# Performance work log

Hardware: AMD Instinct MI355X
Metric: run time of the kernel (lower is better)

Reference implementation:

```python
import jax, jax.numpy as jnp
import numpy as np

B, E, LC, LE, D = 32, 8, 256, 512, 256   # batch, evi_num, claim_len, evidence_len, emb_dim
OUT, H = 128, 1                          # attention hidden dim, head_num
NEG = -1e18


def setup_inputs() -> dict:
    key = jax.random.key(0)
    ks = jax.random.split(key, 8)
    claim = jax.random.normal(ks[0], (B, E, LC, D), jnp.float32)
    evidence = jax.random.normal(ks[1], (B, E, LE, D), jnp.float32)
    claim_len_mask = jax.random.randint(ks[2], (B, E, 1, LC), 0, 2).astype(jnp.int32)
    evidence_len_mask = jax.random.randint(ks[3], (B, E, 1, LE), 0, 2).astype(jnp.int32)
    s2d = 1.0 / np.sqrt(2 * D)
    so = 1.0 / np.sqrt(OUT)
    W1 = jax.random.normal(ks[4], (2 * D, OUT), jnp.float32) * s2d  # torch W1.weight.T
    w2 = jax.random.normal(ks[5], (OUT, H), jnp.float32) * so
    W2 = jax.random.normal(ks[6], (2 * D, OUT), jnp.float32) * s2d
    w1 = jax.random.normal(ks[7], (OUT, H), jnp.float32) * so
    return {"claim": claim, "claim_len_mask": claim_len_mask,
            "evidence": evidence, "evidence_len_mask": evidence_len_mask,
            "W1": W1, "w2": w2, "W2": W2, "w1": w1}


def _pooled_attend(seq, seq_mask, pooled, W, w):
    # seq: (B,E,L,D), pooled: (B,E,1,D), W: (2D,OUT), w: (OUT,H)
    # cat([seq, pooled_expanded]) @ W  ==  seq @ W[:D] + pooled @ W[D:]  (broadcast)
    h = jnp.tanh(seq @ W[:D] + pooled @ W[D:])          # (B,E,L,OUT)
    att = h @ w                                          # (B,E,L,H)
    mask = jnp.swapaxes(seq_mask, -1, -2).astype(bool)   # (B,E,L,1), broadcast over H
    att = jnp.where(mask, att, NEG)
    scores = jax.nn.softmax(att, axis=-2)                # softmax over L
    out = jnp.einsum('belh,beld->behd', scores, seq)     # (B,E,H,D)
    return out.reshape(out.shape[0], out.shape[1], 1, -1)  # (B,E,1,H*D)


def reference(claim, claim_len_mask, evidence, evidence_len_mask, W1, w2, W2, w1):
    c_mean = jnp.mean(claim, axis=-2, keepdims=True)     # (B,E,1,D)
    e_hat = _pooled_attend(evidence, evidence_len_mask, c_mean, W1, w2)
    e_mean = jnp.mean(evidence, axis=-2, keepdims=True)  # (B,E,1,D)
    c_hat = _pooled_attend(claim, claim_len_mask, e_mean, W2, w1)
    return c_hat, e_hat
```

## Files before the change

kernel.cpp:

```cpp
#include <hip/hip_runtime.h>
#include <hip/hip_bf16.h>
#include <math.h>

#define BE   256
#define DIM  256
#define OUTD 128
#define LCL  256
#define LEV  512
#define NEGV -1e18f

typedef short  bf16x8  __attribute__((ext_vector_type(8)));
typedef float  floatx4 __attribute__((ext_vector_type(4)));

union BF1 { __hip_bfloat16 h; unsigned short u; };
union BF2 { __hip_bfloat162 h; unsigned int u; };

__device__ __forceinline__ float fast_tanh(float x) {
    float xc = fminf(fmaxf(x, -15.f), 15.f);
    float e = __expf(2.f * xc);
    return (e - 1.f) * __builtin_amdgcn_rcpf(e + 1.f);
}

__global__ __launch_bounds__(512) void k_meanbias(
    const float* __restrict__ claim, const float* __restrict__ evidence,
    const float* __restrict__ W1, const float* __restrict__ W2,
    float* __restrict__ bias_e, float* __restrict__ bias_c,
    unsigned short* __restrict__ WT1, unsigned short* __restrict__ WT2)
{
    const int bid = blockIdx.x;
    const int t = threadIdx.x;
    if (bid >= BE) {
        const int side = bid - BE;
        const float* W = side ? W2 : W1;
        unsigned short* WT = side ? WT2 : WT1;
        for (int i = t; i < OUTD * DIM; i += 512) {
            const int d = i & (DIM - 1);
            const int n = i >> 8;
            BF1 c; c.h = __float2bfloat16(W[(size_t)d * OUTD + n]);
            WT[n * DIM + d] = c.u;
        }
        return;
    }
    const int pair = bid;
    const int d4 = t & 63, rg = t >> 6;
    __shared__ float4 smc[8][64];
    __shared__ float4 sme[8][64];
    __shared__ float mc[DIM], me[DIM];
    __shared__ float sb[2][2][OUTD];

    const float4* c4 = (const float4*)(claim + (size_t)pair * LCL * DIM);
    const float4* e4 = (const float4*)(evidence + (size_t)pair * LEV * DIM);
    float4 ac = make_float4(0.f, 0.f, 0.f, 0.f);
    float4 ae = make_float4(0.f, 0.f, 0.f, 0.f);
#pragma unroll 4
    for (int r = rg; r < LCL; r += 8) {
        const float4 v = c4[r * 64 + d4];
        ac.x += v.x; ac.y += v.y; ac.z += v.z; ac.w += v.w;
    }
#pragma unroll 4
    for (int r = rg; r < LEV; r += 8) {
        const float4 v = e4[r * 64 + d4];
        ae.x += v.x; ae.y += v.y; ae.z += v.z; ae.w += v.w;
    }
    smc[rg][d4] = ac; sme[rg][d4] = ae;
    __syncthreads();
    if (t < 64) {
        float4 s = make_float4(0.f, 0.f, 0.f, 0.f);
#pragma unroll
        for (int j = 0; j < 8; ++j) {
            const float4 v = smc[j][t];
            s.x += v.x; s.y += v.y; s.z += v.z; s.w += v.w;
        }
        ((float4*)mc)[t] = make_float4(s.x * (1.f / LCL), s.y * (1.f / LCL),
                                       s.z * (1.f / LCL), s.w * (1.f / LCL));
    } else if (t < 128) {
        const int u = t - 64;
        float4 s = make_float4(0.f, 0.f, 0.f, 0.f);
#pragma unroll
        for (int j = 0; j < 8; ++j) {
            const float4 v = sme[j][u];
            s.x += v.x; s.y += v.y; s.z += v.z; s.w += v.w;
        }
        ((float4*)me)[u] = make_float4(s.x * (1.f / LEV), s.y * (1.f / LEV),
                                       s.z * (1.f / LEV), s.w * (1.f / LEV));
    }
    __syncthreads();
    const int side = t >> 8, o = t & 127, dh = (t >> 7) & 1;
    const float* W = side ? W2 : W1;
    const float* m = side ? me : mc;
    float s = 0.f;
#pragma unroll 8
    for (int i = 0; i < 128; ++i) {
        const int d = dh * 128 + i;
        s += m[d] * W[(size_t)(DIM + d) * OUTD + o];
    }
    sb[side][dh][o] = s;
    __syncthreads();
    if (t < 256) {
        const int sd = t >> 7, oo = t & 127;
        const float bv = sb[sd][0][oo] + sb[sd][1][oo];
        (sd ? bias_c : bias_e)[pair * OUTD + oo] = bv;
    }
}

__global__ __launch_bounds__(512, 2) void k_fused(
    const float* __restrict__ claim, const float* __restrict__ evidence,
    const unsigned short* __restrict__ WT1, const unsigned short* __restrict__ WT2,
    const float* __restrict__ w2v, const float* __restrict__ w1v,
    const float* __restrict__ bias_e, const float* __restrict__ bias_c,
    const int* __restrict__ emask, const int* __restrict__ cmask,
    float* __restrict__ out)
{
    constexpr int SR4 = 65;
    __shared__ float4 sA4[64 * SR4];
    __shared__ float sred[64][2];
    __shared__ float patt[64];
    __shared__ float stats[2];

    const int bid = blockIdx.x;
    const bool is_ev = (bid & 1) == 0;
    const int pair = bid >> 1;
    const float* __restrict__ seq  = is_ev ? evidence : claim;
    const unsigned short* __restrict__ WT = is_ev ? WT1 : WT2;
    const float* __restrict__ wvec = is_ev ? w2v : w1v;
    const float* __restrict__ bias = is_ev ? bias_e : bias_c;
    const int*   __restrict__ mask = is_ev ? emask : cmask;
    float* __restrict__ outp       = is_ev ? out + (size_t)BE * DIM : out;
    const int L  = is_ev ? LEV : LCL;
    const int NT = L >> 6;

    const int t = threadIdx.x;
    const int lane = t & 63;
    const int wv = t >> 6;
    const int wrow = wv >> 1;
    const int wcolg = wv & 1;
    const int q = lane >> 4, c16 = lane & 15;
    const int d4 = t & 63, rg = t >> 6;

    float bc[4], wc[4];
#pragma unroll
    for (int ct = 0; ct < 4; ++ct) {
        const int col = wcolg * 64 + ct * 16 + c16;
        bc[ct] = bias[pair * OUTD + col];
        wc[ct] = wvec[col];
    }
    const unsigned short* wbase = WT + (size_t)(wcolg * 64 + c16) * DIM + q * 8;
    const float4* sp4 = (const float4*)(seq + (size_t)pair * L * DIM);

    float4 nx[8];
#pragma unroll
    for (int j = 0; j < 8; ++j) nx[j] = sp4[t + j * 512];
#pragma unroll
    for (int j = 0; j < 8; ++j) {
        const int idx = t + j * 512;
        sA4[(idx >> 6) * SR4 + (idx & 63)] = nx[j];
    }
    __syncthreads();

    float4 Oac = make_float4(0.f, 0.f, 0.f, 0.f);
    float m_run = -INFINITY, l_run = 0.f;

    for (int tile = 0; tile < NT; ++tile) {
        const bool has_nxt = (tile + 1 < NT);
        if (has_nxt) {
            const float4* np4 = sp4 + (size_t)(tile + 1) * 4096;
#pragma unroll
            for (int j = 0; j < 8; ++j) nx[j] = np4[t + j * 512];
        }

        floatx4 acc[4];
#pragma unroll
        for (int ct = 0; ct < 4; ++ct) acc[ct] = (floatx4){0.f, 0.f, 0.f, 0.f};
        const int arow = wrow * 16 + c16;
#pragma unroll
        for (int ks = 0; ks < 8; ++ks) {
            bf16x8 bfr[4];
#pragma unroll
            for (int ct = 0; ct < 4; ++ct)
                bfr[ct] = *(const bf16x8*)(wbase + (size_t)ct * 16 * DIM + ks * 32);
            const float4 lo = sA4[arow * SR4 + ks * 8 + q * 2];
            const float4 hi = sA4[arow * SR4 + ks * 8 + q * 2 + 1];
            union { bf16x8 v; BF2 p[4]; } ua;
            ua.p[0].h = __float22bfloat162_rn(make_float2(lo.x, lo.y));
            ua.p[1].h = __float22bfloat162_rn(make_float2(lo.z, lo.w));
            ua.p[2].h = __float22bfloat162_rn(make_float2(hi.x, hi.y));
            ua.p[3].h = __float22bfloat162_rn(make_float2(hi.z, hi.w));
#pragma unroll
            for (int ct = 0; ct < 4; ++ct)
                acc[ct] = __builtin_amdgcn_mfma_f32_16x16x32_bf16(ua.v, bfr[ct], acc[ct], 0, 0, 0);
        }

#pragma unroll
        for (int reg = 0; reg < 4; ++reg) {
            float s = 0.f;
#pragma unroll
            for (int ct = 0; ct < 4; ++ct)
                s += fast_tanh(acc[ct][reg] + bc[ct]) * wc[ct];
#pragma unroll
            for (int off = 1; off < 16; off <<= 1) s += __shfl_xor(s, off, 64);
            if (c16 == 0)
                sred[wrow * 16 + q * 4 + reg][wcolg] = s;
        }
        __syncthreads();

        if (t < 64) {
            float a = sred[t][0] + sred[t][1];
            a = mask[pair * L + tile * 64 + t] ? a : NEGV;
            float mx = a;
#pragma unroll
            for (int off = 1; off < 64; off <<= 1) mx = fmaxf(mx, __shfl_xor(mx, off, 64));
            const float newm = fmaxf(m_run, mx);
            const float e = expf(a - newm);
            patt[t] = e;
            float sm = e;
#pragma unroll
            for (int off = 1; off < 64; off <<= 1) sm += __shfl_xor(sm, off, 64);
            if (t == 0) { stats[0] = newm; stats[1] = sm; }
        }
        __syncthreads();
        const float newm = stats[0], tsum = stats[1];
        const float scale = expf(m_run - newm);
        l_run = l_run * scale + tsum;
        m_run = newm;
        Oac.x *= scale; Oac.y *= scale; Oac.z *= scale; Oac.w *= scale;

#pragma unroll
        for (int r = 0; r < 8; ++r) {
            const float pl = patt[rg * 8 + r];
            const float4 v = sA4[(rg * 8 + r) * SR4 + d4];
            Oac.x += pl * v.x; Oac.y += pl * v.y; Oac.z += pl * v.z; Oac.w += pl * v.w;
        }

        if (has_nxt) {
            __syncthreads();
#pragma unroll
            for (int j = 0; j < 8; ++j) {
                const int idx = t + j * 512;
                sA4[(idx >> 6) * SR4 + (idx & 63)] = nx[j];
            }
            __syncthreads();
        }
    }

    __syncthreads();
    sA4[t] = Oac;
    __syncthreads();
    if (t < 64) {
        float4 s = make_float4(0.f, 0.f, 0.f, 0.f);
#pragma unroll
        for (int j = 0; j < 8; ++j) {
            const float4 v = sA4[j * 64 + t];
            s.x += v.x; s.y += v.y; s.z += v.z; s.w += v.w;
        }
        const float inv = 1.f / l_run;
        ((float4*)(outp + (size_t)pair * DIM))[t] =
            make_float4(s.x * inv, s.y * inv, s.z * inv, s.w * inv);
    }
}

extern "C" void kernel_launch(void* const* d_in, const int* in_sizes, int n_in,
                              void* d_out, int out_size, void* d_ws, size_t ws_size,
                              hipStream_t stream) {
    const float* claim    = (const float*)d_in[0];
    const int*   cmask    = (const int*)  d_in[1];
    const float* evidence = (const float*)d_in[2];
    const int*   emask    = (const int*)  d_in[3];
    const float* W1       = (const float*)d_in[4];
    const float* w2       = (const float*)d_in[5];
    const float* W2       = (const float*)d_in[6];
    const float* w1       = (const float*)d_in[7];
    float* out = (float*)d_out;

    float* ws = (float*)d_ws;
    float* bias_e = ws;
    float* bias_c = bias_e + BE * OUTD;
    unsigned short* WT1 = (unsigned short*)(bias_c + BE * OUTD);
    unsigned short* WT2 = WT1 + OUTD * DIM;

    k_meanbias<<<BE + 2, 512, 0, stream>>>(claim, evidence, W1, W2,
                                           bias_e, bias_c, WT1, WT2);
    k_fused<<<2 * BE, 512, 0, stream>>>(claim, evidence, WT1, WT2, w2, w1,
                                        bias_e, bias_c, emask, cmask, out);
}
```

Measured before the change: 399.0 us.

## Double-buffer sequence tiles in LDS with direct global-to-LDS async loads

The fused attention kernel now stages each 64-row tile straight into LDS with global_load_lds, 16 bytes per lane. It keeps two LDS buffers so the next tile loads while the current one feeds the MFMA and softmax steps. This replaces the register-staged prefetch and its extra barrier-and-store phase, and it also lowers register use. The cost is that LDS per block roughly doubles and the occupancy hint of two blocks is dropped, so likely only one block fits per CU. The async loads also share the in-order vmcnt counter with the weight loads, which may cut into the overlap. The mean kernel's reduction loops get a larger unroll factor.

New measurement: 349.6 us. 1.14x faster.

```diff
diff --git a/kernel.cpp b/kernel.cpp
--- a/kernel.cpp
+++ b/kernel.cpp
@@ -19,6 +19,13 @@
     float xc = fminf(fmaxf(x, -15.f), 15.f);
     float e = __expf(2.f * xc);
     return (e - 1.f) * __builtin_amdgcn_rcpf(e + 1.f);
+}
+
+__device__ __forceinline__ void gl_lds16(const float4* g, float4* l) {
+    __builtin_amdgcn_global_load_lds(
+        (const __attribute__((address_space(1))) unsigned int*)(const void*)g,
+        (__attribute__((address_space(3))) unsigned int*)(void*)l,
+        16, 0, 0);
 }
 
 __global__ __launch_bounds__(512) void k_meanbias(
@@ -52,12 +59,12 @@
     const float4* e4 = (const float4*)(evidence + (size_t)pair * LEV * DIM);
     float4 ac = make_float4(0.f, 0.f, 0.f, 0.f);
     float4 ae = make_float4(0.f, 0.f, 0.f, 0.f);
-#pragma unroll 4
+#pragma unroll 8
     for (int r = rg; r < LCL; r += 8) {
         const float4 v = c4[r * 64 + d4];
         ac.x += v.x; ac.y += v.y; ac.z += v.z; ac.w += v.w;
     }
-#pragma unroll 4
+#pragma unroll 8
     for (int r = rg; r < LEV; r += 8) {
         const float4 v = e4[r * 64 + d4];
         ae.x += v.x; ae.y += v.y; ae.z += v.z; ae.w += v.w;
@@ -103,7 +110,7 @@
     }
 }
 
-__global__ __launch_bounds__(512, 2) void k_fused(
+__global__ __launch_bounds__(512) void k_fused(
     const float* __restrict__ claim, const float* __restrict__ evidence,
     const unsigned short* __restrict__ WT1, const unsigned short* __restrict__ WT2,
     const float* __restrict__ w2v, const float* __restrict__ w1v,
@@ -112,7 +119,7 @@
     float* __restrict__ out)
 {
     constexpr int SR4 = 65;
-    __shared__ float4 sA4[64 * SR4];
+    __shared__ float4 sA4[2][64 * SR4];
     __shared__ float sred[64][2];
     __shared__ float patt[64];
     __shared__ float stats[2];
@@ -147,26 +154,24 @@
     const unsigned short* wbase = WT + (size_t)(wcolg * 64 + c16) * DIM + q * 8;
     const float4* sp4 = (const float4*)(seq + (size_t)pair * L * DIM);
 
-    float4 nx[8];
-#pragma unroll
-    for (int j = 0; j < 8; ++j) nx[j] = sp4[t + j * 512];
-#pragma unroll
-    for (int j = 0; j < 8; ++j) {
-        const int idx = t + j * 512;
-        sA4[(idx >> 6) * SR4 + (idx & 63)] = nx[j];
-    }
-    __syncthreads();
+    auto stage = [&](int buf, int tile) {
+        const float4* base = sp4 + (size_t)tile * 4096;
+#pragma unroll
+        for (int j = 0; j < 8; ++j) {
+            const int row = wv * 8 + j;
+            gl_lds16(base + row * 64 + lane, &sA4[buf][row * SR4]);
+        }
+    };
+
+    stage(0, 0);
+    int cur = 0;
 
     float4 Oac = make_float4(0.f, 0.f, 0.f, 0.f);
     float m_run = -INFINITY, l_run = 0.f;
 
     for (int tile = 0; tile < NT; ++tile) {
-        const bool has_nxt = (tile + 1 < NT);
-        if (has_nxt) {
-            const float4* np4 = sp4 + (size_t)(tile + 1) * 4096;
-#pragma unroll
-            for (int j = 0; j < 8; ++j) nx[j] = np4[t + j * 512];
-        }
+        __syncthreads();
+        if (tile + 1 < NT) stage(cur ^ 1, tile + 1);
 
         floatx4 acc[4];
 #pragma unroll
@@ -178,8 +183,8 @@
 #pragma unroll
             for (int ct = 0; ct < 4; ++ct)
                 bfr[ct] = *(const bf16x8*)(wbase + (size_t)ct * 16 * DIM + ks * 32);
-            const float4 lo = sA4[arow * SR4 + ks * 8 + q * 2];
-            const float4 hi = sA4[arow * SR4 + ks * 8 + q * 2 + 1];
+            const float4 lo = sA4[cur][arow * SR4 + ks * 8 + q * 2];
+            const float4 hi = sA4[cur][arow * SR4 + ks * 8 + q * 2 + 1];
             union { bf16x8 v; BF2 p[4]; } ua;
             ua.p[0].h = __float22bfloat162_rn(make_float2(lo.x, lo.y));
             ua.p[1].h = __float22bfloat162_rn(make_float2(lo.z, lo.w));
@@ -227,29 +232,20 @@
 #pragma unroll
         for (int r = 0; r < 8; ++r) {
             const float pl = patt[rg * 8 + r];
-            const float4 v = sA4[(rg * 8 + r) * SR4 + d4];
+            const float4 v = sA4[cur][(rg * 8 + r) * SR4 + d4];
             Oac.x += pl * v.x; Oac.y += pl * v.y; Oac.z += pl * v.z; Oac.w += pl * v.w;
         }
-
-        if (has_nxt) {
-            __syncthreads();
-#pragma unroll
-            for (int j = 0; j < 8; ++j) {
-                const int idx = t + j * 512;
-                sA4[(idx >> 6) * SR4 + (idx & 63)] = nx[j];
-            }
-            __syncthreads();
-        }
-    }
-
-    __syncthreads();
-    sA4[t] = Oac;
+        cur ^= 1;
+    }
+
+    __syncthreads();
+    ((float4*)sA4)[t] = Oac;
     __syncthreads();
     if (t < 64) {
         float4 s = make_float4(0.f, 0.f, 0.f, 0.f);
 #pragma unroll
         for (int j = 0; j < 8; ++j) {
-            const float4 v = sA4[j * 64 + t];
+            const float4 v = ((float4*)sA4)[j * 64 + t];
             s.x += v.x; s.y += v.y; s.z += v.z; s.w += v.w;
         }
         const float inv = 1.f / l_run;
```
